# Kernel tuning notes

Hardware: AMD Instinct MI355X
Metric: run time of the kernel (lower is better)

## Reference

```python
import jax, jax.numpy as jnp
import numpy as np

EPS = 1e-7  # keras.backend.epsilon()


def setup_inputs() -> dict:
    key = jax.random.key(0)
    k1, k2 = jax.random.split(key)
    B, S, D = 8, 1024, 768
    # scale down: module exponentiates raw dot products with no max-subtraction
    input_a = jax.random.normal(k1, (B, S, D), dtype=jnp.float32) * 0.05
    input_mask = jax.random.randint(k2, (B, S), 0, 2, dtype=jnp.int32)
    return {"input_a": input_a, "input_mask": input_mask}


def reference(input_a, input_mask):
    # e = exp(Q K^T) with Q = K = input_a, attend_type='dot' (no scaling)
    e = jnp.exp(jnp.einsum('bsd,btd->bst', input_a, input_a))  # [B,S,S]
    m = input_mask.astype(input_a.dtype)
    e = e * m[:, :, None] * m[:, None, :]  # mask rows and cols
    e = e / (jnp.sum(e, axis=-1, keepdims=True) + EPS)  # renormalize
    attend = jnp.einsum('bst,btd->bsd', e, input_a)  # V = input_a
    return attend
```

## Files before the change

### kernel.cpp

```cpp
#include <hip/hip_runtime.h>
#include <cstdint>
#include <cstddef>

#define BATCH 8
#define SEQ 1024
#define DIM 768
#define EPS_K 1e-7f

typedef __bf16 bf16x8 __attribute__((ext_vector_type(8)));
typedef float f32x16 __attribute__((ext_vector_type(16)));
typedef uint16_t u16x8 __attribute__((ext_vector_type(8)));

#define MFMA32(a, b, c) __builtin_amdgcn_mfma_f32_32x32x16_bf16((a), (b), (c), 0, 0, 0)

__device__ __forceinline__ uint16_t f2bf(float f) {
  union { float f; uint32_t u; } v; v.f = f;
  uint32_t u = v.u;
  u += 0x7FFFu + ((u >> 16) & 1u);
  return (uint16_t)(u >> 16);
}

__device__ __forceinline__ void gload16(const void* g, void* l) {
  __builtin_amdgcn_global_load_lds(
      (const __attribute__((address_space(1))) uint32_t*)g,
      (__attribute__((address_space(3))) uint32_t*)l, 16, 0, 0);
}

__global__ __launch_bounds__(256) void convert_kernel(const float* __restrict__ A,
                                                      uint16_t* __restrict__ ab,
                                                      uint16_t* __restrict__ at) {
  const int b  = blockIdx.z;
  const int s0 = blockIdx.y * 64;
  const int d0 = blockIdx.x * 64;
  __shared__ uint16_t tl[64][80];
  const int tid = threadIdx.x;
#pragma unroll
  for (int i = 0; i < 2; ++i) {
    const int sl = (tid >> 3) + i * 32;
    const int ch = tid & 7;
    const float* src = A + ((size_t)b * SEQ + s0 + sl) * DIM + d0 + ch * 8;
    float4 f0 = *(const float4*)src;
    float4 f1 = *(const float4*)(src + 4);
    u16x8 h;
    h[0] = f2bf(f0.x); h[1] = f2bf(f0.y); h[2] = f2bf(f0.z); h[3] = f2bf(f0.w);
    h[4] = f2bf(f1.x); h[5] = f2bf(f1.y); h[6] = f2bf(f1.z); h[7] = f2bf(f1.w);
    *(u16x8*)&ab[((size_t)b * SEQ + s0 + sl) * DIM + d0 + ch * 8] = h;
    *(u16x8*)&tl[sl][ch * 8] = h;
  }
  __syncthreads();
  const int dl = tid >> 2;
#pragma unroll
  for (int i = 0; i < 2; ++i) {
    const int sc = (tid & 3) + i * 4;
    u16x8 h;
#pragma unroll
    for (int e = 0; e < 8; ++e) h[e] = tl[sc * 8 + e][dl];
    *(u16x8*)&at[((size_t)b * DIM + d0 + dl) * SEQ + s0 + sc * 8] = h;
  }
}


__global__ __launch_bounds__(256) void scores_kernel(const uint16_t* __restrict__ ab,
                                                     const int* __restrict__ mask,
                                                     uint16_t* __restrict__ P) {
  const int b    = blockIdx.x & 7;
  const int tile = blockIdx.x >> 3;
  const int s0   = (tile >> 3) * 128;
  const int t0   = (tile & 7) * 128;

  const int tid  = threadIdx.x;
  const int lane = tid & 63;
  const int l31  = lane & 31;
  const int lhi  = lane >> 5;
  const int wid  = tid >> 6;
  const int wr   = wid >> 1;
  const int wc   = wid & 1;

  __shared__ __align__(16) uint16_t lQ[2][128 * 32];
  __shared__ __align__(16) uint16_t lK[2][128 * 32];
  __shared__ float mrow[128];
  __shared__ float mcol[128];

  if (tid < 128)        mrow[tid]       = (float)mask[b * SEQ + s0 + tid];
  else                  mcol[tid - 128] = (float)mask[b * SEQ + t0 + (tid - 128)];

  const uint16_t* gQ = ab + ((size_t)b * SEQ + s0) * DIM;
  const uint16_t* gK = ab + ((size_t)b * SEQ + t0) * DIM;

  const int strow = tid >> 2;
  const int schx  = (((tid & 3) ^ ((tid >> 3) & 3)) << 3);
  const int sdst  = tid * 8;
#define STG(L, G, LDG, buf, k0)                                                \
  { gload16(G + (size_t)strow * (LDG) + (k0) + schx, &L[buf][sdst]);           \
    gload16(G + (size_t)(strow + 64) * (LDG) + (k0) + schx,                    \
            &L[buf][sdst + 2048]); }

  f32x16 acc[2][2];
#pragma unroll
  for (int m = 0; m < 2; ++m)
#pragma unroll
    for (int n = 0; n < 2; ++n)
#pragma unroll
      for (int r = 0; r < 16; ++r) acc[m][n][r] = 0.f;

  int offQ[2][2], offK[2][2];
#pragma unroll
  for (int m = 0; m < 2; ++m) {
    const int rQ = wr * 64 + m * 32 + l31;
    const int rK = wc * 64 + m * 32 + l31;
#pragma unroll
    for (int kk = 0; kk < 2; ++kk) {
      offQ[m][kk] = rQ * 32 + (((kk << 1) + lhi) ^ ((rQ >> 1) & 3)) * 8;
      offK[m][kk] = rK * 32 + (((kk << 1) + lhi) ^ ((rK >> 1) & 3)) * 8;
    }
  }

  STG(lQ, gQ, DIM, 0, 0); STG(lK, gK, DIM, 0, 0);
  __syncthreads();

  const int NT = DIM / 32;
  int cur = 0;
  for (int t = 0; t < NT; ++t) {
    const int nx = cur ^ 1;
    if (t + 1 < NT) { STG(lQ, gQ, DIM, nx, (t + 1) * 32); STG(lK, gK, DIM, nx, (t + 1) * 32); }

    bf16x8 qf[2][2], kf[2][2];
#pragma unroll
    for (int m = 0; m < 2; ++m)
#pragma unroll
      for (int kk = 0; kk < 2; ++kk) {
        qf[m][kk] = *(const bf16x8*)&lQ[cur][offQ[m][kk]];
        kf[m][kk] = *(const bf16x8*)&lK[cur][offK[m][kk]];
      }
#pragma unroll
    for (int kk = 0; kk < 2; ++kk)
#pragma unroll
      for (int m = 0; m < 2; ++m)
#pragma unroll
        for (int n = 0; n < 2; ++n)
          acc[m][n] = MFMA32(qf[m][kk], kf[n][kk], acc[m][n]);

    __syncthreads();
    cur ^= 1;
  }

  uint16_t* Pb = P + (size_t)b * SEQ * SEQ;
#pragma unroll
  for (int m = 0; m < 2; ++m) {
#pragma unroll
    for (int n = 0; n < 2; ++n) {
      const int cl = wc * 64 + n * 32 + l31;
      const float mc = mcol[cl];
#pragma unroll
      for (int r = 0; r < 16; ++r) {
        const int rl = wr * 64 + m * 32 + (r & 3) + 8 * (r >> 2) + 4 * lhi;
        float e = __expf(acc[m][n][r]) * mrow[rl] * mc;
        Pb[(size_t)(s0 + rl) * SEQ + t0 + cl] = f2bf(e);
      }
    }
  }
}

__global__ __launch_bounds__(256) void out_kernel(const uint16_t* __restrict__ P,
                                                  const uint16_t* __restrict__ at,
                                                  float* __restrict__ out) {
  const int b    = blockIdx.x & 7;
  const int tile = blockIdx.x >> 3;
  const int q0   = (tile / 6) * 128;
  const int d0   = (tile % 6) * 128;

  const int tid  = threadIdx.x;
  const int lane = tid & 63;
  const int l31  = lane & 31;
  const int lhi  = lane >> 5;
  const int wid  = tid >> 6;
  const int wr   = wid >> 1;
  const int wc   = wid & 1;

  __shared__ __align__(16) uint16_t lP[2][128 * 32];
  __shared__ __align__(16) uint16_t lV[2][128 * 32];

  const uint16_t* gP = P  + ((size_t)b * SEQ + q0) * SEQ;
  const uint16_t* gV = at + ((size_t)b * DIM + d0) * SEQ;

  const int strow = tid >> 2;
  const int schx  = (((tid & 3) ^ ((tid >> 3) & 3)) << 3);
  const int sdst  = tid * 8;

  f32x16 acc[2][2];
  f32x16 accd[2];
#pragma unroll
  for (int m = 0; m < 2; ++m) {
#pragma unroll
    for (int r = 0; r < 16; ++r) accd[m][r] = 0.f;
#pragma unroll
    for (int n = 0; n < 2; ++n)
#pragma unroll
      for (int r = 0; r < 16; ++r) acc[m][n][r] = 0.f;
  }
  bf16x8 ones;
#pragma unroll
  for (int i = 0; i < 8; ++i) ones[i] = (__bf16)1.0f;

  int offP[2][2], offV[2][2];
#pragma unroll
  for (int m = 0; m < 2; ++m) {
    const int rP = wr * 64 + m * 32 + l31;
    const int rV = wc * 64 + m * 32 + l31;
#pragma unroll
    for (int kk = 0; kk < 2; ++kk) {
      offP[m][kk] = rP * 32 + (((kk << 1) + lhi) ^ ((rP >> 1) & 3)) * 8;
      offV[m][kk] = rV * 32 + (((kk << 1) + lhi) ^ ((rV >> 1) & 3)) * 8;
    }
  }

  STG(lP, gP, SEQ, 0, 0); STG(lV, gV, SEQ, 0, 0);
  __syncthreads();

  const int NT = SEQ / 32;
  int cur = 0;
  for (int t = 0; t < NT; ++t) {
    const int nx = cur ^ 1;
    if (t + 1 < NT) { STG(lP, gP, SEQ, nx, (t + 1) * 32); STG(lV, gV, SEQ, nx, (t + 1) * 32); }

    bf16x8 pf[2][2], vf[2][2];
#pragma unroll
    for (int m = 0; m < 2; ++m)
#pragma unroll
      for (int kk = 0; kk < 2; ++kk) {
        pf[m][kk] = *(const bf16x8*)&lP[cur][offP[m][kk]];
        vf[m][kk] = *(const bf16x8*)&lV[cur][offV[m][kk]];
      }
#pragma unroll
    for (int kk = 0; kk < 2; ++kk)
#pragma unroll
      for (int m = 0; m < 2; ++m) {
#pragma unroll
        for (int n = 0; n < 2; ++n)
          acc[m][n] = MFMA32(pf[m][kk], vf[n][kk], acc[m][n]);
        accd[m] = MFMA32(pf[m][kk], ones, accd[m]);
      }

    __syncthreads();
    cur ^= 1;
  }

  float* ob = out + (size_t)b * SEQ * DIM;
#pragma unroll
  for (int m = 0; m < 2; ++m) {
#pragma unroll
    for (int r = 0; r < 16; ++r) {
      const int rl = wr * 64 + m * 32 + (r & 3) + 8 * (r >> 2) + 4 * lhi;
      const float sc = 1.0f / (accd[m][r] + EPS_K);
#pragma unroll
      for (int n = 0; n < 2; ++n) {
        const int d = d0 + wc * 64 + n * 32 + l31;
        ob[(size_t)(q0 + rl) * DIM + d] = acc[m][n][r] * sc;
      }
    }
  }
}
#undef STG

extern "C" void kernel_launch(void* const* d_in, const int* in_sizes, int n_in,
                              void* d_out, int out_size, void* d_ws, size_t ws_size,
                              hipStream_t stream) {
  (void)in_sizes; (void)n_in; (void)out_size; (void)ws_size;
  const float* A    = (const float*)d_in[0];
  const int*   mask = (const int*)d_in[1];
  float*       out  = (float*)d_out;

  char* ws = (char*)d_ws;
  const size_t NB_AB = (size_t)BATCH * SEQ * DIM * 2;
  const size_t NB_AT = NB_AB;
  uint16_t* ab = (uint16_t*)(ws);
  uint16_t* at = (uint16_t*)(ws + NB_AB);
  uint16_t* P  = (uint16_t*)(ws + NB_AB + NB_AT);

  convert_kernel<<<dim3(DIM / 64, SEQ / 64, BATCH), dim3(256), 0, stream>>>(A, ab, at);
  scores_kernel<<<dim3(64 * BATCH), dim3(256), 0, stream>>>(ab, mask, P);
  out_kernel<<<dim3(48 * BATCH), dim3(256), 0, stream>>>(P, at, out);
}
```

Measured before the change: 126.7 us.

## Switch to 16x16x32 MFMA with 128x64 tiles to double grid size

```diff
diff --git a/kernel.cpp b/kernel.cpp
--- a/kernel.cpp
+++ b/kernel.cpp
@@ -8,10 +8,10 @@
 #define EPS_K 1e-7f
 
 typedef __bf16 bf16x8 __attribute__((ext_vector_type(8)));
-typedef float f32x16 __attribute__((ext_vector_type(16)));
+typedef float f32x4 __attribute__((ext_vector_type(4)));
 typedef uint16_t u16x8 __attribute__((ext_vector_type(8)));
 
-#define MFMA32(a, b, c) __builtin_amdgcn_mfma_f32_32x32x16_bf16((a), (b), (c), 0, 0, 0)
+#define MFMA16(a, b, c) __builtin_amdgcn_mfma_f32_16x16x32_bf16((a), (b), (c), 0, 0, 0)
 
 __device__ __forceinline__ uint16_t f2bf(float f) {
   union { float f; uint32_t u; } v; v.f = f;
@@ -65,97 +65,80 @@
                                                      uint16_t* __restrict__ P) {
   const int b    = blockIdx.x & 7;
   const int tile = blockIdx.x >> 3;
-  const int s0   = (tile >> 3) * 128;
-  const int t0   = (tile & 7) * 128;
+  const int s0   = (tile >> 4) * 128;
+  const int t0   = (tile & 15) * 64;
 
   const int tid  = threadIdx.x;
   const int lane = tid & 63;
-  const int l31  = lane & 31;
-  const int lhi  = lane >> 5;
   const int wid  = tid >> 6;
   const int wr   = wid >> 1;
   const int wc   = wid & 1;
 
   __shared__ __align__(16) uint16_t lQ[2][128 * 32];
-  __shared__ __align__(16) uint16_t lK[2][128 * 32];
+  __shared__ __align__(16) uint16_t lK[2][64 * 32];
   __shared__ float mrow[128];
-  __shared__ float mcol[128];
-
-  if (tid < 128)        mrow[tid]       = (float)mask[b * SEQ + s0 + tid];
-  else                  mcol[tid - 128] = (float)mask[b * SEQ + t0 + (tid - 128)];
+  __shared__ float mcol[64];
+
+  if (tid < 128)                  mrow[tid]       = (float)mask[b * SEQ + s0 + tid];
+  else if (tid < 192)             mcol[tid - 128] = (float)mask[b * SEQ + t0 + (tid - 128)];
 
   const uint16_t* gQ = ab + ((size_t)b * SEQ + s0) * DIM;
   const uint16_t* gK = ab + ((size_t)b * SEQ + t0) * DIM;
 
   const int strow = tid >> 2;
-  const int schx  = (((tid & 3) ^ ((tid >> 3) & 3)) << 3);
+  const int sch   = (tid & 3) * 8;
   const int sdst  = tid * 8;
-#define STG(L, G, LDG, buf, k0)                                                \
-  { gload16(G + (size_t)strow * (LDG) + (k0) + schx, &L[buf][sdst]);           \
-    gload16(G + (size_t)(strow + 64) * (LDG) + (k0) + schx,                    \
-            &L[buf][sdst + 2048]); }
-
-  f32x16 acc[2][2];
-#pragma unroll
-  for (int m = 0; m < 2; ++m)
-#pragma unroll
-    for (int n = 0; n < 2; ++n)
-#pragma unroll
-      for (int r = 0; r < 16; ++r) acc[m][n][r] = 0.f;
-
-  int offQ[2][2], offK[2][2];
-#pragma unroll
-  for (int m = 0; m < 2; ++m) {
-    const int rQ = wr * 64 + m * 32 + l31;
-    const int rK = wc * 64 + m * 32 + l31;
-#pragma unroll
-    for (int kk = 0; kk < 2; ++kk) {
-      offQ[m][kk] = rQ * 32 + (((kk << 1) + lhi) ^ ((rQ >> 1) & 3)) * 8;
-      offK[m][kk] = rK * 32 + (((kk << 1) + lhi) ^ ((rK >> 1) & 3)) * 8;
-    }
-  }
-
-  STG(lQ, gQ, DIM, 0, 0); STG(lK, gK, DIM, 0, 0);
+#define STG(buf, k0)                                                           \
+  { gload16(gQ + (size_t)strow * DIM + (k0) + sch, &lQ[buf][sdst]);            \
+    gload16(gQ + (size_t)(strow + 64) * DIM + (k0) + sch, &lQ[buf][sdst + 2048]); \
+    gload16(gK + (size_t)strow * DIM + (k0) + sch, &lK[buf][sdst]); }
+
+  f32x4 acc[4][2];
+#pragma unroll
+  for (int m = 0; m < 4; ++m)
+#pragma unroll
+    for (int n = 0; n < 2; ++n) acc[m][n] = f32x4{0.f, 0.f, 0.f, 0.f};
+
+  const int rQ  = wr * 64 + (lane & 15);
+  const int rK  = wc * 32 + (lane & 15);
+  const int kch = (lane >> 4) * 8;
+
+  STG(0, 0);
   __syncthreads();
 
   const int NT = DIM / 32;
   int cur = 0;
   for (int t = 0; t < NT; ++t) {
-    const int nx = cur ^ 1;
-    if (t + 1 < NT) { STG(lQ, gQ, DIM, nx, (t + 1) * 32); STG(lK, gK, DIM, nx, (t + 1) * 32); }
-
-    bf16x8 qf[2][2], kf[2][2];
-#pragma unroll
-    for (int m = 0; m < 2; ++m)
-#pragma unroll
-      for (int kk = 0; kk < 2; ++kk) {
-        qf[m][kk] = *(const bf16x8*)&lQ[cur][offQ[m][kk]];
-        kf[m][kk] = *(const bf16x8*)&lK[cur][offK[m][kk]];
-      }
-#pragma unroll
-    for (int kk = 0; kk < 2; ++kk)
-#pragma unroll
-      for (int m = 0; m < 2; ++m)
-#pragma unroll
-        for (int n = 0; n < 2; ++n)
-          acc[m][n] = MFMA32(qf[m][kk], kf[n][kk], acc[m][n]);
+    if (t + 1 < NT) STG(cur ^ 1, (t + 1) * 32);
+
+    bf16x8 qf[4], kf[2];
+#pragma unroll
+    for (int m = 0; m < 4; ++m) qf[m] = *(const bf16x8*)&lQ[cur][(rQ + m * 16) * 32 + kch];
+#pragma unroll
+    for (int n = 0; n < 2; ++n) kf[n] = *(const bf16x8*)&lK[cur][(rK + n * 16) * 32 + kch];
+#pragma unroll
+    for (int m = 0; m < 4; ++m)
+#pragma unroll
+      for (int n = 0; n < 2; ++n)
+        acc[m][n] = MFMA16(qf[m], kf[n], acc[m][n]);
 
     __syncthreads();
     cur ^= 1;
   }
+#undef STG
 
   uint16_t* Pb = P + (size_t)b * SEQ * SEQ;
 #pragma unroll
-  for (int m = 0; m < 2; ++m) {
+  for (int m = 0; m < 4; ++m) {
+    const int qb = wr * 64 + m * 16 + (lane >> 4) * 4;
 #pragma unroll
     for (int n = 0; n < 2; ++n) {
-      const int cl = wc * 64 + n * 32 + l31;
-      const float mc = mcol[cl];
-#pragma unroll
-      for (int r = 0; r < 16; ++r) {
-        const int rl = wr * 64 + m * 32 + (r & 3) + 8 * (r >> 2) + 4 * lhi;
-        float e = __expf(acc[m][n][r]) * mrow[rl] * mc;
-        Pb[(size_t)(s0 + rl) * SEQ + t0 + cl] = f2bf(e);
+      const int tl = wc * 32 + n * 16 + (lane & 15);
+      const float mc = mcol[tl];
+#pragma unroll
+      for (int j = 0; j < 4; ++j) {
+        float e = __expf(acc[m][n][j]) * mrow[qb + j] * mc;
+        Pb[(size_t)(s0 + qb + j) * SEQ + t0 + tl] = f2bf(e);
       }
     }
   }
@@ -166,101 +149,86 @@
                                                   float* __restrict__ out) {
   const int b    = blockIdx.x & 7;
   const int tile = blockIdx.x >> 3;
-  const int q0   = (tile / 6) * 128;
-  const int d0   = (tile % 6) * 128;
+  const int q0   = (tile / 12) * 128;
+  const int d0   = (tile % 12) * 64;
 
   const int tid  = threadIdx.x;
   const int lane = tid & 63;
-  const int l31  = lane & 31;
-  const int lhi  = lane >> 5;
   const int wid  = tid >> 6;
   const int wr   = wid >> 1;
   const int wc   = wid & 1;
 
   __shared__ __align__(16) uint16_t lP[2][128 * 32];
-  __shared__ __align__(16) uint16_t lV[2][128 * 32];
+  __shared__ __align__(16) uint16_t lV[2][64 * 32];
 
   const uint16_t* gP = P  + ((size_t)b * SEQ + q0) * SEQ;
   const uint16_t* gV = at + ((size_t)b * DIM + d0) * SEQ;
 
   const int strow = tid >> 2;
-  const int schx  = (((tid & 3) ^ ((tid >> 3) & 3)) << 3);
+  const int sch   = (tid & 3) * 8;
   const int sdst  = tid * 8;
-
-  f32x16 acc[2][2];
-  f32x16 accd[2];
-#pragma unroll
-  for (int m = 0; m < 2; ++m) {
-#pragma unroll
-    for (int r = 0; r < 16; ++r) accd[m][r] = 0.f;
-#pragma unroll
-    for (int n = 0; n < 2; ++n)
-#pragma unroll
-      for (int r = 0; r < 16; ++r) acc[m][n][r] = 0.f;
+#define STG(buf, k0)                                                           \
+  { gload16(gP + (size_t)strow * SEQ + (k0) + sch, &lP[buf][sdst]);            \
+    gload16(gP + (size_t)(strow + 64) * SEQ + (k0) + sch, &lP[buf][sdst + 2048]); \
+    gload16(gV + (size_t)strow * SEQ + (k0) + sch, &lV[buf][sdst]); }
+
+  f32x4 acc[4][2];
+  f32x4 accd[4];
+#pragma unroll
+  for (int m = 0; m < 4; ++m) {
+    accd[m] = f32x4{0.f, 0.f, 0.f, 0.f};
+#pragma unroll
+    for (int n = 0; n < 2; ++n) acc[m][n] = f32x4{0.f, 0.f, 0.f, 0.f};
   }
   bf16x8 ones;
 #pragma unroll
   for (int i = 0; i < 8; ++i) ones[i] = (__bf16)1.0f;
 
-  int offP[2][2], offV[2][2];
-#pragma unroll
-  for (int m = 0; m < 2; ++m) {
-    const int rP = wr * 64 + m * 32 + l31;
-    const int rV = wc * 64 + m * 32 + l31;
-#pragma unroll
-    for (int kk = 0; kk < 2; ++kk) {
-      offP[m][kk] = rP * 32 + (((kk << 1) + lhi) ^ ((rP >> 1) & 3)) * 8;
-      offV[m][kk] = rV * 32 + (((kk << 1) + lhi) ^ ((rV >> 1) & 3)) * 8;
-    }
-  }
-
-  STG(lP, gP, SEQ, 0, 0); STG(lV, gV, SEQ, 0, 0);
+  const int rP  = wr * 64 + (lane & 15);
+  const int rV  = wc * 32 + (lane & 15);
+  const int kch = (lane >> 4) * 8;
+
+  STG(0, 0);
   __syncthreads();
 
   const int NT = SEQ / 32;
   int cur = 0;
   for (int t = 0; t < NT; ++t) {
-    const int nx = cur ^ 1;
-    if (t + 1 < NT) { STG(lP, gP, SEQ, nx, (t + 1) * 32); STG(lV, gV, SEQ, nx, (t + 1) * 32); }
-
-    bf16x8 pf[2][2], vf[2][2];
-#pragma unroll
-    for (int m = 0; m < 2; ++m)
-#pragma unroll
-      for (int kk = 0; kk < 2; ++kk) {
-        pf[m][kk] = *(const bf16x8*)&lP[cur][offP[m][kk]];
-        vf[m][kk] = *(const bf16x8*)&lV[cur][offV[m][kk]];
-      }
-#pragma unroll
-    for (int kk = 0; kk < 2; ++kk)
-#pragma unroll
-      for (int m = 0; m < 2; ++m) {
-#pragma unroll
-        for (int n = 0; n < 2; ++n)
-          acc[m][n] = MFMA32(pf[m][kk], vf[n][kk], acc[m][n]);
-        accd[m] = MFMA32(pf[m][kk], ones, accd[m]);
-      }
+    if (t + 1 < NT) STG(cur ^ 1, (t + 1) * 32);
+
+    bf16x8 pf[4], vf[2];
+#pragma unroll
+    for (int m = 0; m < 4; ++m) pf[m] = *(const bf16x8*)&lP[cur][(rP + m * 16) * 32 + kch];
+#pragma unroll
+    for (int n = 0; n < 2; ++n) vf[n] = *(const bf16x8*)&lV[cur][(rV + n * 16) * 32 + kch];
+#pragma unroll
+    for (int m = 0; m < 4; ++m) {
+#pragma unroll
+      for (int n = 0; n < 2; ++n)
+        acc[m][n] = MFMA16(pf[m], vf[n], acc[m][n]);
+      accd[m] = MFMA16(pf[m], ones, accd[m]);
+    }
 
     __syncthreads();
     cur ^= 1;
   }
+#undef STG
 
   float* ob = out + (size_t)b * SEQ * DIM;
 #pragma unroll
-  for (int m = 0; m < 2; ++m) {
-#pragma unroll
-    for (int r = 0; r < 16; ++r) {
-      const int rl = wr * 64 + m * 32 + (r & 3) + 8 * (r >> 2) + 4 * lhi;
-      const float sc = 1.0f / (accd[m][r] + EPS_K);
+  for (int m = 0; m < 4; ++m) {
+#pragma unroll
+    for (int j = 0; j < 4; ++j) {
+      const int q  = q0 + wr * 64 + m * 16 + (lane >> 4) * 4 + j;
+      const float sc = 1.0f / (accd[m][j] + EPS_K);
 #pragma unroll
       for (int n = 0; n < 2; ++n) {
-        const int d = d0 + wc * 64 + n * 32 + l31;
-        ob[(size_t)(q0 + rl) * DIM + d] = acc[m][n][r] * sc;
+        const int d = d0 + wc * 32 + n * 16 + (lane & 15);
+        ob[(size_t)q * DIM + d] = acc[m][n][j] * sc;
       }
     }
   }
 }
-#undef STG
 
 extern "C" void kernel_launch(void* const* d_in, const int* in_sizes, int n_in,
                               void* d_out, int out_size, void* d_ws, size_t ws_size,
@@ -278,6 +246,6 @@
   uint16_t* P  = (uint16_t*)(ws + NB_AB + NB_AT);
 
   convert_kernel<<<dim3(DIM / 64, SEQ / 64, BATCH), dim3(256), 0, stream>>>(A, ab, at);
-  scores_kernel<<<dim3(64 * BATCH), dim3(256), 0, stream>>>(ab, mask, P);
-  out_kernel<<<dim3(48 * BATCH), dim3(256), 0, stream>>>(P, at, out);
-}
+  scores_kernel<<<dim3(128 * BATCH), dim3(256), 0, stream>>>(ab, mask, P);
+  out_kernel<<<dim3(96 * BATCH), dim3(256), 0, stream>>>(P, at, out);
+}
```

Measured after the change: 131.1 us. 3.5% more time.
